# Kernel tuning notes

Measured on AMD Instinct MI355X. Metric: run time of the kernel, lower is better.

## Reference

```python
import jax, jax.numpy as jnp
import numpy as np

N, E, IN, H, G, OUT = 50000, 800000, 128, 128, 64, 10
HEADS, C = 4, 32  # per-head dim = H // HEADS so 4-head concat -> H (keeps chain dims consistent)


def setup_inputs() -> dict:
    key = jax.random.key(0)
    ks = jax.random.split(key, 16)
    p = lambda i, shape: jax.random.normal(ks[i], shape, jnp.float32) * 0.05
    return {
        "x": jax.random.normal(ks[0], (N, IN), jnp.float32),
        "edge_index": jax.random.randint(ks[1], (2, E), 0, N),
        "batch": jnp.sort(jax.random.randint(ks[2], (N,), 0, G)),
        "gcn_W": p(3, (IN, H)), "gcn_b": jnp.zeros((H,), jnp.float32),
        "gat_W": p(4, (H, HEADS * C)),
        "att_src": p(5, (HEADS, C)), "att_dst": p(6, (HEADS, C)),
        "gat_b": jnp.zeros((HEADS * C,), jnp.float32),
        "ec_W1": p(7, (2 * H, 128)), "ec_b1": jnp.zeros((128,), jnp.float32),
        "ec_W2": p(8, (128, H)), "ec_b2": jnp.zeros((H,), jnp.float32),
        "gin_W1": p(9, (H, 128)), "gin_b1": jnp.zeros((128,), jnp.float32),
        "gin_W2": p(10, (128, H)), "gin_b2": jnp.zeros((H,), jnp.float32),
        "gate_W1": p(11, (H, 128)), "gate_b1": jnp.zeros((128,), jnp.float32),
        "gate_W2": p(12, (128, 1)), "gate_b2": jnp.zeros((1,), jnp.float32),
        "fc_W": p(13, (H, OUT)), "fc_b": jnp.zeros((OUT,), jnp.float32),
    }


def reference(x, edge_index, batch, gcn_W, gcn_b, gat_W, att_src, att_dst, gat_b,
              ec_W1, ec_b1, ec_W2, ec_b2, gin_W1, gin_b1, gin_W2, gin_b2,
              gate_W1, gate_b1, gate_W2, gate_b2, fc_W, fc_b):
    src, dst = edge_index[0], edge_index[1]
    loop = jnp.arange(N)
    src_l = jnp.concatenate([src, loop])  # self loops for GCN / GAT
    dst_l = jnp.concatenate([dst, loop])

    deg = jax.ops.segment_sum(jnp.ones_like(dst_l, jnp.float32), dst_l, N)
    dinv = jnp.where(deg > 0, jax.lax.rsqrt(deg), 0.0)
    h = x @ gcn_W
    norm = dinv[src_l] * dinv[dst_l]  # [E+N]
    h = jax.ops.segment_sum(h[src_l] * norm[:, None], dst_l, N) + gcn_b
    h = jax.nn.relu(h)

    # ---- GATConv: 4 heads, per-target edge softmax, concat ----
    g = (h @ gat_W).reshape(N, HEADS, C)
    a_src = (g * att_src).sum(-1)  # [N, HEADS]
    a_dst = (g * att_dst).sum(-1)
    e = jax.nn.leaky_relu(a_src[src_l] + a_dst[dst_l], 0.2)  # [E+N, HEADS]
    e_max = jax.ops.segment_max(e, dst_l, N)
    e = jnp.exp(e - e_max[dst_l])
    e_sum = jax.ops.segment_sum(e, dst_l, N)
    alpha = e / (e_sum[dst_l] + 1e-16)
    h = jax.ops.segment_sum(g[src_l] * alpha[..., None], dst_l, N).reshape(N, HEADS * C) + gat_b
    h = jax.nn.elu(h)

    # ---- EdgeConv: nn([x_i, x_j - x_i]) with max aggregation ----
    msg = jnp.concatenate([h[dst], h[src] - h[dst]], axis=-1)  # [E, 2H]
    msg = jax.nn.relu(msg @ ec_W1 + ec_b1) @ ec_W2 + ec_b2
    agg = jax.ops.segment_max(msg, dst, N)
    h = jax.nn.relu(jnp.where(jnp.isfinite(agg), agg, 0.0))  # isolated nodes -> 0 (PyG scatter-max fill)

    # ---- GINConv (eps=0): nn(x + sum_j x_j) ----
    s = h + jax.ops.segment_sum(h[src], dst, N)
    h = jax.nn.relu(jax.nn.relu(s @ gin_W1 + gin_b1) @ gin_W2 + gin_b2)

    # ---- GlobalAttention pooling: per-graph softmax gating ----
    gate = jax.nn.relu(h @ gate_W1 + gate_b1) @ gate_W2 + gate_b2  # [N, 1]
    gmax = jax.ops.segment_max(gate, batch, G)
    ge = jnp.exp(gate - gmax[batch])
    gsum = jax.ops.segment_sum(ge, batch, G)
    w = ge / (gsum[batch] + 1e-16)
    pooled = jax.ops.segment_sum(w * h, batch, G)  # [G, H]

    out = pooled @ fc_W + fc_b
    return jax.nn.log_softmax(out, axis=1)
```

## Files before the change

### kernel.cpp

```cpp
#include <hip/hip_runtime.h>

#define H 128
#define OUTD 10

typedef short bf16x8 __attribute__((ext_vector_type(8)));
typedef float f32x4 __attribute__((ext_vector_type(4)));

__device__ __forceinline__ unsigned short f2bf(float x) {
  unsigned u = __float_as_uint(x);
  u += 0x7fffu + ((u >> 16) & 1u);
  return (unsigned short)(u >> 16);
}
__device__ __forceinline__ unsigned pack2bf(float a, float b) {
  return (unsigned)f2bf(a) | ((unsigned)f2bf(b) << 16);
}
__device__ __forceinline__ float bf2f(unsigned short u) {
  return __uint_as_float(((unsigned)u) << 16);
}
__device__ __forceinline__ float bflo(unsigned u) { return __uint_as_float(u << 16); }
__device__ __forceinline__ float bfhi(unsigned u) { return __uint_as_float(u & 0xffff0000u); }

__device__ __forceinline__ unsigned fenc(float x) {
  unsigned u = __float_as_uint(x);
  return (u & 0x80000000u) ? ~u : (u | 0x80000000u);
}
__device__ __forceinline__ float fdec(unsigned u) {
  u = (u & 0x80000000u) ? (u & 0x7fffffffu) : ~u;
  return __uint_as_float(u);
}

__global__ void prep_w(const float* __restrict__ gcnW, const float* __restrict__ gatW,
                       const float* __restrict__ ecW1, const float* __restrict__ ecW2,
                       const float* __restrict__ ginW1, const float* __restrict__ ginW2,
                       const float* __restrict__ gtW1, unsigned short* __restrict__ WT) {
  int f = blockIdx.x * 256 + threadIdx.x;
  if (f >= 8 * 16384) return;
  int m = f >> 14, idx = f & 16383;
  int j = idx >> 7, k = idx & 127;
  int src = k * 128 + j;
  float v;
  switch (m) {
    case 0: v = gcnW[src]; break;
    case 1: v = gatW[src]; break;
    case 2: v = ecW1[src] - ecW1[16384 + src]; break;
    case 3: v = ecW1[16384 + src]; break;
    case 4: v = ecW2[src]; break;
    case 5: v = ginW1[src]; break;
    case 6: v = ginW2[src]; break;
    default: v = gtW1[src]; break;
  }
  WT[f] = f2bf(v);
}

template <int IN_BF, int RELU, int BIAS>
__global__ __launch_bounds__(256) void dense_mfma(const void* __restrict__ Xv,
                                                  const unsigned short* __restrict__ WT,
                                                  const float* __restrict__ bias,
                                                  unsigned short* __restrict__ Y, int n) {
  __shared__ unsigned short tile[64][136];
  const int tid = threadIdx.x, lane = tid & 63, wave = tid >> 6;
  const int jl = lane & 15, kg = lane >> 4;
  const int base = blockIdx.x * 64;
  if (base >= n) return;
  const int nr = min(64, n - base);
  if (IN_BF) {
    const uint4* X4 = (const uint4*)Xv;
#pragma unroll
    for (int it = 0; it < 4; ++it) {
      int f = it * 256 + tid, r = f >> 4, q = f & 15;
      if (r < nr) *(uint4*)&tile[r][q * 8] = X4[(size_t)(base + r) * 16 + q];
    }
  } else {
    const float* X = (const float*)Xv;
#pragma unroll
    for (int it = 0; it < 16; ++it) {
      int f = it * 256 + tid, r = f >> 6, kp = f & 63;
      if (r < nr) {
        float2 v = *(const float2*)&X[(size_t)(base + r) * H + 2 * kp];
        *(unsigned*)&tile[r][2 * kp] = pack2bf(v.x, v.y);
      }
    }
  }
  __syncthreads();
  bf16x8 afrag[4];
#pragma unroll
  for (int kk = 0; kk < 4; ++kk)
    afrag[kk] = *(const bf16x8*)&tile[wave * 16 + jl][kk * 32 + kg * 8];
  f32x4 acc[8];
#pragma unroll
  for (int jt = 0; jt < 8; ++jt) {
    f32x4 c = {0.f, 0.f, 0.f, 0.f};
#pragma unroll
    for (int kk = 0; kk < 4; ++kk) {
      bf16x8 bf = *(const bf16x8*)&WT[(size_t)(jt * 16 + jl) * H + kk * 32 + kg * 8];
      c = __builtin_amdgcn_mfma_f32_16x16x32_bf16(afrag[kk], bf, c, 0, 0, 0);
    }
    if (BIAS) {
      float bb = bias[jt * 16 + jl];
#pragma unroll
      for (int r = 0; r < 4; ++r) c[r] += bb;
    }
    if (RELU) {
#pragma unroll
      for (int r = 0; r < 4; ++r) c[r] = fmaxf(c[r], 0.f);
    }
    acc[jt] = c;
  }
  __syncthreads();
#pragma unroll
  for (int jt = 0; jt < 8; ++jt)
#pragma unroll
    for (int r = 0; r < 4; ++r) tile[wave * 16 + kg * 4 + r][jt * 16 + jl] = f2bf(acc[jt][r]);
  __syncthreads();
#pragma unroll
  for (int it = 0; it < 4; ++it) {
    int f = it * 256 + tid, r = f >> 4, q = f & 15;
    if (r < nr) *(uint4*)&Y[(size_t)(base + r) * H + q * 8] = *(const uint4*)&tile[r][q * 8];
  }
}

__global__ __launch_bounds__(256) void dense_dual(const unsigned short* __restrict__ X,
                                                  const unsigned short* __restrict__ WT1,
                                                  const unsigned short* __restrict__ WT2,
                                                  const float* __restrict__ bias2,
                                                  unsigned short* __restrict__ Y1,
                                                  unsigned short* __restrict__ Y2, int n) {
  __shared__ unsigned short tile[64][136];
  const int tid = threadIdx.x, lane = tid & 63, wave = tid >> 6;
  const int jl = lane & 15, kg = lane >> 4;
  const int base = blockIdx.x * 64;
  if (base >= n) return;
  const int nr = min(64, n - base);
  const uint4* X4 = (const uint4*)X;
#pragma unroll
  for (int it = 0; it < 4; ++it) {
    int f = it * 256 + tid, r = f >> 4, q = f & 15;
    if (r < nr) *(uint4*)&tile[r][q * 8] = X4[(size_t)(base + r) * 16 + q];
  }
  __syncthreads();
  bf16x8 afrag[4];
#pragma unroll
  for (int kk = 0; kk < 4; ++kk)
    afrag[kk] = *(const bf16x8*)&tile[wave * 16 + jl][kk * 32 + kg * 8];
  f32x4 acc[8];
#pragma unroll
  for (int jt = 0; jt < 8; ++jt) {
    f32x4 c = {0.f, 0.f, 0.f, 0.f};
#pragma unroll
    for (int kk = 0; kk < 4; ++kk) {
      bf16x8 bf = *(const bf16x8*)&WT1[(size_t)(jt * 16 + jl) * H + kk * 32 + kg * 8];
      c = __builtin_amdgcn_mfma_f32_16x16x32_bf16(afrag[kk], bf, c, 0, 0, 0);
    }
    acc[jt] = c;
  }
  __syncthreads();
#pragma unroll
  for (int jt = 0; jt < 8; ++jt)
#pragma unroll
    for (int r = 0; r < 4; ++r) tile[wave * 16 + kg * 4 + r][jt * 16 + jl] = f2bf(acc[jt][r]);
  __syncthreads();
#pragma unroll
  for (int it = 0; it < 4; ++it) {
    int f = it * 256 + tid, r = f >> 4, q = f & 15;
    if (r < nr) *(uint4*)&Y1[(size_t)(base + r) * H + q * 8] = *(const uint4*)&tile[r][q * 8];
  }
  __syncthreads();
#pragma unroll
  for (int jt = 0; jt < 8; ++jt) {
    f32x4 c = {0.f, 0.f, 0.f, 0.f};
#pragma unroll
    for (int kk = 0; kk < 4; ++kk) {
      bf16x8 bf = *(const bf16x8*)&WT2[(size_t)(jt * 16 + jl) * H + kk * 32 + kg * 8];
      c = __builtin_amdgcn_mfma_f32_16x16x32_bf16(afrag[kk], bf, c, 0, 0, 0);
    }
    float bb = bias2[jt * 16 + jl];
#pragma unroll
    for (int r = 0; r < 4; ++r) c[r] += bb;
    acc[jt] = c;
  }
  __syncthreads();
#pragma unroll
  for (int jt = 0; jt < 8; ++jt)
#pragma unroll
    for (int r = 0; r < 4; ++r) tile[wave * 16 + kg * 4 + r][jt * 16 + jl] = f2bf(acc[jt][r]);
  __syncthreads();
#pragma unroll
  for (int it = 0; it < 4; ++it) {
    int f = it * 256 + tid, r = f >> 4, q = f & 15;
    if (r < nr) *(uint4*)&Y2[(size_t)(base + r) * H + q * 8] = *(const uint4*)&tile[r][q * 8];
  }
}

__global__ __launch_bounds__(256) void dense_chain(const unsigned short* __restrict__ X,
                                                   const unsigned short* __restrict__ WT1,
                                                   const float* __restrict__ b1,
                                                   const unsigned short* __restrict__ WT2,
                                                   const float* __restrict__ b2,
                                                   unsigned short* __restrict__ Y, int n) {
  __shared__ unsigned short tile[64][136];
  const int tid = threadIdx.x, lane = tid & 63, wave = tid >> 6;
  const int jl = lane & 15, kg = lane >> 4;
  const int base = blockIdx.x * 64;
  if (base >= n) return;
  const int nr = min(64, n - base);
  const uint4* X4 = (const uint4*)X;
#pragma unroll
  for (int it = 0; it < 4; ++it) {
    int f = it * 256 + tid, r = f >> 4, q = f & 15;
    if (r < nr) *(uint4*)&tile[r][q * 8] = X4[(size_t)(base + r) * 16 + q];
  }
  __syncthreads();
  bf16x8 af[4];
#pragma unroll
  for (int kk = 0; kk < 4; ++kk) af[kk] = *(const bf16x8*)&tile[wave * 16 + jl][kk * 32 + kg * 8];
  f32x4 acc[8];
#pragma unroll
  for (int jt = 0; jt < 8; ++jt) {
    f32x4 c = {0.f, 0.f, 0.f, 0.f};
#pragma unroll
    for (int kk = 0; kk < 4; ++kk) {
      bf16x8 bf = *(const bf16x8*)&WT1[(size_t)(jt * 16 + jl) * H + kk * 32 + kg * 8];
      c = __builtin_amdgcn_mfma_f32_16x16x32_bf16(af[kk], bf, c, 0, 0, 0);
    }
    float bb = b1[jt * 16 + jl];
#pragma unroll
    for (int r = 0; r < 4; ++r) c[r] = fmaxf(c[r] + bb, 0.f);
    acc[jt] = c;
  }
  __syncthreads();
#pragma unroll
  for (int jt = 0; jt < 8; ++jt)
#pragma unroll
    for (int r = 0; r < 4; ++r) tile[wave * 16 + kg * 4 + r][jt * 16 + jl] = f2bf(acc[jt][r]);
  __syncthreads();
#pragma unroll
  for (int kk = 0; kk < 4; ++kk) af[kk] = *(const bf16x8*)&tile[wave * 16 + jl][kk * 32 + kg * 8];
#pragma unroll
  for (int jt = 0; jt < 8; ++jt) {
    f32x4 c = {0.f, 0.f, 0.f, 0.f};
#pragma unroll
    for (int kk = 0; kk < 4; ++kk) {
      bf16x8 bf = *(const bf16x8*)&WT2[(size_t)(jt * 16 + jl) * H + kk * 32 + kg * 8];
      c = __builtin_amdgcn_mfma_f32_16x16x32_bf16(af[kk], bf, c, 0, 0, 0);
    }
    float bb = b2[jt * 16 + jl];
#pragma unroll
    for (int r = 0; r < 4; ++r) c[r] = fmaxf(c[r] + bb, 0.f);
    acc[jt] = c;
  }
  __syncthreads();
#pragma unroll
  for (int jt = 0; jt < 8; ++jt)
#pragma unroll
    for (int r = 0; r < 4; ++r) tile[wave * 16 + kg * 4 + r][jt * 16 + jl] = f2bf(acc[jt][r]);
  __syncthreads();
#pragma unroll
  for (int it = 0; it < 4; ++it) {
    int f = it * 256 + tid, r = f >> 4, q = f & 15;
    if (r < nr) *(uint4*)&Y[(size_t)(base + r) * H + q * 8] = *(const uint4*)&tile[r][q * 8];
  }
}

__global__ __launch_bounds__(256) void dense_gate(const unsigned short* __restrict__ X,
                                                  const unsigned short* __restrict__ WT,
                                                  const float* __restrict__ b1,
                                                  const float* __restrict__ w2,
                                                  const float* __restrict__ b2,
                                                  float* __restrict__ gate, int n) {
  __shared__ unsigned short tile[64][136];
  const int tid = threadIdx.x, lane = tid & 63, wave = tid >> 6;
  const int jl = lane & 15, kg = lane >> 4;
  const int base = blockIdx.x * 64;
  if (base >= n) return;
  const int nr = min(64, n - base);
  const uint4* X4 = (const uint4*)X;
#pragma unroll
  for (int it = 0; it < 4; ++it) {
    int f = it * 256 + tid, r = f >> 4, q = f & 15;
    if (r < nr) *(uint4*)&tile[r][q * 8] = X4[(size_t)(base + r) * 16 + q];
  }
  __syncthreads();
  bf16x8 af[4];
#pragma unroll
  for (int kk = 0; kk < 4; ++kk) af[kk] = *(const bf16x8*)&tile[wave * 16 + jl][kk * 32 + kg * 8];
  float p0 = 0.f, p1 = 0.f, p2 = 0.f, p3 = 0.f;
#pragma unroll
  for (int jt = 0; jt < 8; ++jt) {
    f32x4 c = {0.f, 0.f, 0.f, 0.f};
#pragma unroll
    for (int kk = 0; kk < 4; ++kk) {
      bf16x8 bf = *(const bf16x8*)&WT[(size_t)(jt * 16 + jl) * H + kk * 32 + kg * 8];
      c = __builtin_amdgcn_mfma_f32_16x16x32_bf16(af[kk], bf, c, 0, 0, 0);
    }
    float bb = b1[jt * 16 + jl];
    float wv = w2[jt * 16 + jl];
    p0 = fmaf(fmaxf(c[0] + bb, 0.f), wv, p0);
    p1 = fmaf(fmaxf(c[1] + bb, 0.f), wv, p1);
    p2 = fmaf(fmaxf(c[2] + bb, 0.f), wv, p2);
    p3 = fmaf(fmaxf(c[3] + bb, 0.f), wv, p3);
  }
#pragma unroll
  for (int off = 1; off <= 8; off <<= 1) {
    p0 += __shfl_xor(p0, off);
    p1 += __shfl_xor(p1, off);
    p2 += __shfl_xor(p2, off);
    p3 += __shfl_xor(p3, off);
  }
  if (jl == 0) {
    float bb2 = b2[0];
    int row = wave * 16 + kg * 4;
    if (row + 0 < nr) gate[base + row + 0] = p0 + bb2;
    if (row + 1 < nr) gate[base + row + 1] = p1 + bb2;
    if (row + 2 < nr) gate[base + row + 2] = p2 + bb2;
    if (row + 3 < nr) gate[base + row + 3] = p3 + bb2;
  }
}

__global__ void zero_int(int* p, int n) {
  int i = blockIdx.x * 256 + threadIdx.x;
  if (i < n) p[i] = 0;
}
__global__ void csr_count(const int* __restrict__ ei, int* __restrict__ cnt, int E) {
  int e = blockIdx.x * 256 + threadIdx.x;
  if (e < E) atomicAdd(&cnt[ei[(size_t)E + e]], 1);
}
__global__ __launch_bounds__(1024) void scan50k(const int* __restrict__ cnt,
                                                int* __restrict__ row_ptr, int n) {
  __shared__ int ls[1024];
  int t = threadIdx.x;
  int chunk = (n + 1023) >> 10;
  int a = t * chunk;
  if (a > n) a = n;
  int b = a + chunk;
  if (b > n) b = n;
  int s = 0;
  for (int i = a; i < b; ++i) s += cnt[i];
  ls[t] = s;
  __syncthreads();
  for (int off = 1; off < 1024; off <<= 1) {
    int v = (t >= off) ? ls[t - off] : 0;
    __syncthreads();
    ls[t] += v;
    __syncthreads();
  }
  int run = (t > 0) ? ls[t - 1] : 0;
  for (int i = a; i < b; ++i) {
    row_ptr[i] = run;
    run += cnt[i];
  }
  if (t == 1023) row_ptr[n] = ls[1023];
}
__global__ void copy_int(const int* __restrict__ a, int* __restrict__ b, int n) {
  int i = blockIdx.x * 256 + threadIdx.x;
  if (i < n) b[i] = a[i];
}
__global__ void csr_fill(const int* __restrict__ ei, int* __restrict__ cursor,
                         int* __restrict__ csr_src, int* __restrict__ csr_dst, int E) {
  int e = blockIdx.x * 256 + threadIdx.x;
  if (e >= E) return;
  int s = ei[e], d = ei[(size_t)E + e];
  int p = atomicAdd(&cursor[d], 1);
  csr_src[p] = s;
  csr_dst[p] = d;
}
__global__ void dinv_kernel(const int* __restrict__ row_ptr, float* __restrict__ dinv, int n) {
  int i = blockIdx.x * 256 + threadIdx.x;
  if (i < n) dinv[i] = rsqrtf((float)(1 + row_ptr[i + 1] - row_ptr[i]));
}
__global__ void fill_u32(unsigned* p, unsigned v, size_t n) {
  size_t i = (size_t)blockIdx.x * 256 + threadIdx.x;
  if (i < n) p[i] = v;
}

__global__ __launch_bounds__(256) void gcn_gather(const unsigned short* __restrict__ h,
                                                  const float* __restrict__ dinv,
                                                  const int* __restrict__ row_ptr,
                                                  const int* __restrict__ csr_src,
                                                  const float* __restrict__ bias,
                                                  unsigned short* __restrict__ out, int n) {
  int node = blockIdx.x * 4 + (threadIdx.x >> 6);
  int lane = threadIdx.x & 63;
  if (node >= n) return;
  const unsigned* hu = (const unsigned*)h;
  float di = dinv[node];
  unsigned v = hu[(size_t)node * 64 + lane];
  float t0 = bflo(v) * di, t1 = bfhi(v) * di;
  int a = row_ptr[node], b = row_ptr[node + 1];
  int e = a;
  for (; e + 8 <= b; e += 8) {
    int sx[8];
#pragma unroll
    for (int i = 0; i < 8; ++i) sx[i] = csr_src[e + i];
    unsigned w[8];
    float dd[8];
#pragma unroll
    for (int i = 0; i < 8; ++i) w[i] = hu[(size_t)sx[i] * 64 + lane];
#pragma unroll
    for (int i = 0; i < 8; ++i) dd[i] = dinv[sx[i]];
#pragma unroll
    for (int i = 0; i < 8; ++i) {
      t0 = fmaf(bflo(w[i]), dd[i], t0);
      t1 = fmaf(bfhi(w[i]), dd[i], t1);
    }
  }
  for (; e < b; ++e) {
    int s = csr_src[e];
    float ds = dinv[s];
    unsigned w = hu[(size_t)s * 64 + lane];
    t0 = fmaf(bflo(w), ds, t0);
    t1 = fmaf(bfhi(w), ds, t1);
  }
  float y0 = fmaxf(fmaf(t0, di, bias[lane * 2]), 0.f);
  float y1 = fmaxf(fmaf(t1, di, bias[lane * 2 + 1]), 0.f);
  ((unsigned*)out)[(size_t)node * 64 + lane] = pack2bf(y0, y1);
}

__global__ void att_pre(const unsigned short* __restrict__ g, const float* __restrict__ attS,
                        const float* __restrict__ attD, float* __restrict__ asrc,
                        float* __restrict__ adst, int n) {
  int t = blockIdx.x * 256 + threadIdx.x;
  if (t >= n * 4) return;
  int i = t >> 2, hd = t & 3;
  const unsigned* gr = (const unsigned*)(g + (size_t)i * H + hd * 32);
  float s1 = 0.f, s2 = 0.f;
#pragma unroll
  for (int p = 0; p < 16; ++p) {
    unsigned u = gr[p];
    float a = bflo(u), b = bfhi(u);
    s1 = fmaf(a, attS[hd * 32 + 2 * p], fmaf(b, attS[hd * 32 + 2 * p + 1], s1));
    s2 = fmaf(a, attD[hd * 32 + 2 * p], fmaf(b, attD[hd * 32 + 2 * p + 1], s2));
  }
  asrc[t] = s1;
  adst[t] = s2;
}

__device__ __forceinline__ float lrelu_exp(float v) {
  v = v > 0.f ? v : 0.2f * v;
  return __expf(v);
}

__global__ __launch_bounds__(256) void gat_gather(const unsigned short* __restrict__ g,
                                                  const float* __restrict__ asrc,
                                                  const float* __restrict__ adst,
                                                  const int* __restrict__ row_ptr,
                                                  const int* __restrict__ csr_src,
                                                  const float* __restrict__ bias,
                                                  unsigned short* __restrict__ out, int n) {
  int node = blockIdx.x * 4 + (threadIdx.x >> 6);
  int lane = threadIdx.x & 63;
  if (node >= n) return;
  const int hd = lane >> 4;
  const unsigned* gu = (const unsigned*)g;
  float adc = adst[node * 4 + hd];
  float w = lrelu_exp(asrc[node * 4 + hd] + adc);
  unsigned u = gu[(size_t)node * 64 + lane];
  float acc0 = w * bflo(u), acc1 = w * bfhi(u), wsum = w;
  int a = row_ptr[node], b = row_ptr[node + 1];
  int e = a;
  for (; e + 4 <= b; e += 4) {
    int s0 = csr_src[e], s1 = csr_src[e + 1], s2 = csr_src[e + 2], s3 = csr_src[e + 3];
    unsigned u0 = gu[(size_t)s0 * 64 + lane], u1 = gu[(size_t)s1 * 64 + lane];
    unsigned u2 = gu[(size_t)s2 * 64 + lane], u3 = gu[(size_t)s3 * 64 + lane];
    float w0 = lrelu_exp(asrc[s0 * 4 + hd] + adc), w1 = lrelu_exp(asrc[s1 * 4 + hd] + adc);
    float w2 = lrelu_exp(asrc[s2 * 4 + hd] + adc), w3 = lrelu_exp(asrc[s3 * 4 + hd] + adc);
    acc0 = fmaf(w0, bflo(u0), acc0);
    acc1 = fmaf(w0, bfhi(u0), acc1);
    acc0 = fmaf(w1, bflo(u1), acc0);
    acc1 = fmaf(w1, bfhi(u1), acc1);
    acc0 = fmaf(w2, bflo(u2), acc0);
    acc1 = fmaf(w2, bfhi(u2), acc1);
    acc0 = fmaf(w3, bflo(u3), acc0);
    acc1 = fmaf(w3, bfhi(u3), acc1);
    wsum += w0 + w1 + w2 + w3;
  }
  for (; e < b; ++e) {
    int s = csr_src[e];
    unsigned us = gu[(size_t)s * 64 + lane];
    float we = lrelu_exp(asrc[s * 4 + hd] + adc);
    acc0 = fmaf(we, bflo(us), acc0);
    acc1 = fmaf(we, bfhi(us), acc1);
    wsum += we;
  }
  float inv = 1.f / (wsum + 1e-16f);
  float r0 = acc0 * inv + bias[2 * lane];
  float r1 = acc1 * inv + bias[2 * lane + 1];
  r0 = r0 > 0.f ? r0 : expm1f(r0);
  r1 = r1 > 0.f ? r1 : expm1f(r1);
  ((unsigned*)out)[(size_t)node * 64 + lane] = pack2bf(r0, r1);
}

__global__ __launch_bounds__(256) void edgeconv_tile(const unsigned short* __restrict__ A,
                                                     const unsigned short* __restrict__ Bm,
                                                     const int* __restrict__ csr_src,
                                                     const int* __restrict__ csr_dst,
                                                     const unsigned short* __restrict__ W2T,
                                                     const float* __restrict__ b2,
                                                     unsigned* __restrict__ hec, int E) {
  __shared__ unsigned short buf[2][64][136];
  __shared__ int dbuf[2][64];
  const int tid = threadIdx.x, lane = tid & 63, wave = tid >> 6;
  const int jl = lane & 15, kg = lane >> 4;
  const int srow = tid >> 2, sq = tid & 3;
  float b2v[8];
#pragma unroll
  for (int jt = 0; jt < 8; ++jt) b2v[jt] = b2[jt * 16 + jl];

  const int tiles = (E + 63) >> 6;
  int t = blockIdx.x;
  if (t >= tiles) return;
  int cur = 0;
  {
    int base = t << 6;
    int ne = min(64, E - base);
    uint2 pk[8];
    if (srow < ne) {
      int d = csr_dst[base + srow], s = csr_src[base + srow];
      const uint2* Ar = (const uint2*)(A + (size_t)d * H + sq * 32);
      const uint2* Br = (const uint2*)(Bm + (size_t)s * H + sq * 32);
#pragma unroll
      for (int i = 0; i < 8; ++i) {
        uint2 va = Ar[i], vb = Br[i];
        pk[i].x = pack2bf(fmaxf(bflo(va.x) + bflo(vb.x), 0.f), fmaxf(bfhi(va.x) + bfhi(vb.x), 0.f));
        pk[i].y = pack2bf(fmaxf(bflo(va.y) + bflo(vb.y), 0.f), fmaxf(bfhi(va.y) + bfhi(vb.y), 0.f));
      }
    } else {
#pragma unroll
      for (int i = 0; i < 8; ++i) pk[i] = {0u, 0u};
    }
#pragma unroll
    for (int i = 0; i < 8; ++i) *(uint2*)&buf[0][srow][sq * 32 + i * 4] = pk[i];
    if (sq == 0) dbuf[0][srow] = (srow < ne) ? csr_dst[base + srow] : -1;
  }
  __syncthreads();

  for (; t < tiles; t += gridDim.x) {
    const int nt = t + gridDim.x;
    const bool havenext = nt < tiles;
    uint2 pk[8];
    if (havenext) {
      int base = nt << 6;
      int ne = min(64, E - base);
      if (srow < ne) {
        int d = csr_dst[base + srow], s = csr_src[base + srow];
        const uint2* Ar = (const uint2*)(A + (size_t)d * H + sq * 32);
        const uint2* Br = (const uint2*)(Bm + (size_t)s * H + sq * 32);
#pragma unroll
        for (int i = 0; i < 8; ++i) {
          uint2 va = Ar[i], vb = Br[i];
          pk[i].x =
              pack2bf(fmaxf(bflo(va.x) + bflo(vb.x), 0.f), fmaxf(bfhi(va.x) + bfhi(vb.x), 0.f));
          pk[i].y =
              pack2bf(fmaxf(bflo(va.y) + bflo(vb.y), 0.f), fmaxf(bfhi(va.y) + bfhi(vb.y), 0.f));
        }
      } else {
#pragma unroll
        for (int i = 0; i < 8; ++i) pk[i] = {0u, 0u};
      }
    }
    bf16x8 af[4];
#pragma unroll
    for (int kk = 0; kk < 4; ++kk)
      af[kk] = *(const bf16x8*)&buf[cur][wave * 16 + jl][kk * 32 + kg * 8];
    const int r0 = wave * 16 + kg * 4;
    const int d0 = dbuf[cur][r0 + 0], d1 = dbuf[cur][r0 + 1];
    const int d2 = dbuf[cur][r0 + 2], d3 = dbuf[cur][r0 + 3];
#pragma unroll
    for (int jt = 0; jt < 8; ++jt) {
      f32x4 c = {0.f, 0.f, 0.f, 0.f};
#pragma unroll
      for (int kk = 0; kk < 4; ++kk) {
        bf16x8 wf = *(const bf16x8*)&W2T[(size_t)(jt * 16 + jl) * H + kk * 32 + kg * 8];
        c = __builtin_amdgcn_mfma_f32_16x16x32_bf16(af[kk], wf, c, 0, 0, 0);
      }
      const int col = jt * 16 + jl;
      int cd = d0;
      float m = c[0];
      if (d1 != cd) {
        if (cd >= 0) atomicMax(&hec[(size_t)cd * H + col], fenc(m + b2v[jt]));
        cd = d1;
        m = c[1];
      } else
        m = fmaxf(m, c[1]);
      if (d2 != cd) {
        if (cd >= 0) atomicMax(&hec[(size_t)cd * H + col], fenc(m + b2v[jt]));
        cd = d2;
        m = c[2];
      } else
        m = fmaxf(m, c[2]);
      if (d3 != cd) {
        if (cd >= 0) atomicMax(&hec[(size_t)cd * H + col], fenc(m + b2v[jt]));
        cd = d3;
        m = c[3];
      } else
        m = fmaxf(m, c[3]);
      if (cd >= 0) atomicMax(&hec[(size_t)cd * H + col], fenc(m + b2v[jt]));
    }
    if (havenext) {
      int base = nt << 6;
      int ne = min(64, E - base);
#pragma unroll
      for (int i = 0; i < 8; ++i) *(uint2*)&buf[cur ^ 1][srow][sq * 32 + i * 4] = pk[i];
      if (sq == 0) dbuf[cur ^ 1][srow] = (srow < ne) ? csr_dst[base + srow] : -1;
    }
    __syncthreads();
    cur ^= 1;
  }
}

__global__ __launch_bounds__(256) void gin_gather(const unsigned* __restrict__ hec,
                                                  const int* __restrict__ row_ptr,
                                                  const int* __restrict__ csr_src,
                                                  unsigned short* __restrict__ out, int n) {
  int node = blockIdx.x * 4 + (threadIdx.x >> 6);
  int lane = threadIdx.x & 63;
  if (node >= n) return;
  uint2 v = *(const uint2*)&hec[(size_t)node * H + lane * 2];
  float t0 = fdec(v.x), t1 = fdec(v.y);
  int a = row_ptr[node], b = row_ptr[node + 1];
  int e = a;
  for (; e + 4 <= b; e += 4) {
    int s0 = csr_src[e], s1 = csr_src[e + 1], s2 = csr_src[e + 2], s3 = csr_src[e + 3];
    uint2 w0 = *(const uint2*)&hec[(size_t)s0 * H + lane * 2];
    uint2 w1 = *(const uint2*)&hec[(size_t)s1 * H + lane * 2];
    uint2 w2 = *(const uint2*)&hec[(size_t)s2 * H + lane * 2];
    uint2 w3 = *(const uint2*)&hec[(size_t)s3 * H + lane * 2];
    t0 += fdec(w0.x) + fdec(w1.x) + fdec(w2.x) + fdec(w3.x);
    t1 += fdec(w0.y) + fdec(w1.y) + fdec(w2.y) + fdec(w3.y);
  }
  for (; e < b; ++e) {
    int s = csr_src[e];
    uint2 w = *(const uint2*)&hec[(size_t)s * H + lane * 2];
    t0 += fdec(w.x);
    t1 += fdec(w.y);
  }
  ((unsigned*)out)[(size_t)node * 64 + lane] = pack2bf(t0, t1);
}

__global__ void starts_kernel(const int* __restrict__ batch, int* __restrict__ starts, int n,
                              int G) {
  int i = blockIdx.x * 256 + threadIdx.x;
  if (i >= n) return;
  int b = batch[i];
  int bp = (i == 0) ? -1 : batch[i - 1];
  for (int g = bp + 1; g <= b; ++g) starts[g] = i;
  if (i == n - 1)
    for (int g = b + 1; g <= G; ++g) starts[g] = n;
}
__global__ __launch_bounds__(256) void pool_fused(float* __restrict__ gate,
                                                  const unsigned short* __restrict__ h4,
                                                  const int* __restrict__ starts,
                                                  const float* __restrict__ fcW,
                                                  const float* __restrict__ fcB,
                                                  float* __restrict__ out) {
  __shared__ float red[256];
  __shared__ float pl[128];
  int g = blockIdx.x, t = threadIdx.x;
  int s0 = starts[g], s1 = starts[g + 1];
  float m = -1e30f;
  for (int i = s0 + t; i < s1; i += 256) m = fmaxf(m, gate[i]);
  red[t] = m;
  __syncthreads();
  for (int off = 128; off; off >>= 1) {
    if (t < off) red[t] = fmaxf(red[t], red[t + off]);
    __syncthreads();
  }
  m = red[0];
  __syncthreads();
  float sm = 0.f;
  for (int i = s0 + t; i < s1; i += 256) {
    float ge = __expf(gate[i] - m);
    gate[i] = ge;
    sm += ge;
  }
  red[t] = sm;
  __syncthreads();
  for (int off = 128; off; off >>= 1) {
    if (t < off) red[t] += red[t + off];
    __syncthreads();
  }
  float inv = 1.f / (red[0] + 1e-16f);
  __syncthreads();
  int c = t & 127, half = t >> 7;
  float acc = 0.f;
  for (int i = s0 + half; i < s1; i += 2) acc = fmaf(gate[i], bf2f(h4[(size_t)i * H + c]), acc);
  red[t] = acc;
  __syncthreads();
  if (t < 128) pl[t] = (red[t] + red[t + 128]) * inv;
  __syncthreads();
  if (t < OUTD) {
    float o = fcB[t];
    for (int k = 0; k < 128; ++k) o = fmaf(pl[k], fcW[k * OUTD + t], o);
    red[t] = o;
  }
  __syncthreads();
  if (t == 0) {
    float mm = -1e30f;
    for (int j = 0; j < OUTD; ++j) mm = fmaxf(mm, red[j]);
    float s = 0.f;
    for (int j = 0; j < OUTD; ++j) s += __expf(red[j] - mm);
    float l = logf(s);
    for (int j = 0; j < OUTD; ++j) out[g * OUTD + j] = red[j] - mm - l;
  }
}

extern "C" void kernel_launch(void* const* d_in, const int* in_sizes, int n_in, void* d_out,
                              int out_size, void* d_ws, size_t ws_size, hipStream_t stream) {
  const float* x = (const float*)d_in[0];
  const int* ei = (const int*)d_in[1];
  const int* batch = (const int*)d_in[2];
  const float* gcnW = (const float*)d_in[3];
  const float* gcnB = (const float*)d_in[4];
  const float* gatW = (const float*)d_in[5];
  const float* attS = (const float*)d_in[6];
  const float* attD = (const float*)d_in[7];
  const float* gatB = (const float*)d_in[8];
  const float* ecW1 = (const float*)d_in[9];
  const float* ecB1 = (const float*)d_in[10];
  const float* ecW2 = (const float*)d_in[11];
  const float* ecB2 = (const float*)d_in[12];
  const float* ginW1 = (const float*)d_in[13];
  const float* ginB1 = (const float*)d_in[14];
  const float* ginW2 = (const float*)d_in[15];
  const float* ginB2 = (const float*)d_in[16];
  const float* gtW1 = (const float*)d_in[17];
  const float* gtB1 = (const float*)d_in[18];
  const float* gtW2 = (const float*)d_in[19];
  const float* gtB2 = (const float*)d_in[20];
  const float* fcW = (const float*)d_in[21];
  const float* fcB = (const float*)d_in[22];

  const int N = in_sizes[0] / H;
  const int E = in_sizes[1] / 2;
  const int G = out_size / OUTD;
  const size_t NH = (size_t)N * H;

  auto align16 = [](char* p) { return (char*)(((uintptr_t)p + 15) & ~(uintptr_t)15); };
  char* p = (char*)d_ws;
  unsigned* hec = (unsigned*)p;      p += NH * 4;
  float* dinv = (float*)p;           p += (size_t)N * 4;
  float* asrc = (float*)p;           p += (size_t)4 * N * 4;
  float* adst = (float*)p;           p += (size_t)4 * N * 4;
  float* gate = (float*)p;           p += (size_t)N * 4;
  int* starts = (int*)p;             p += (size_t)(G + 1) * 4;
  int* cnt = (int*)p;                p += (size_t)N * 4;
  int* row_ptr = (int*)p;            p += (size_t)(N + 1) * 4;
  int* cursor = (int*)p;             p += (size_t)N * 4;
  int* csr_src = (int*)p;            p += (size_t)E * 4;
  int* csr_dst = (int*)p;            p += (size_t)E * 4;
  p = align16(p);
  unsigned short* WT = (unsigned short*)p;  p += (size_t)8 * 16384 * 2;
  p = align16(p);
  unsigned short* T0 = (unsigned short*)p;  p += NH * 2;
  p = align16(p);
  unsigned short* T1 = (unsigned short*)p;  p += NH * 2;
  p = align16(p);
  unsigned short* T2 = (unsigned short*)p;  p += NH * 2;

  const unsigned short* gcnT = WT;
  const unsigned short* gatT = WT + 16384;
  const unsigned short* WaT = WT + 2 * 16384;
  const unsigned short* WbT = WT + 3 * 16384;
  const unsigned short* W2T = WT + 4 * 16384;
  const unsigned short* gin1T = WT + 5 * 16384;
  const unsigned short* gin2T = WT + 6 * 16384;
  const unsigned short* gt1T = WT + 7 * 16384;

  const int gN = (N + 255) / 256;
  const int gNH = (int)((NH + 255) / 256);
  const int gE = (E + 255) / 256;
  const int gDense = (N + 63) / 64;
  const int gW4 = (N + 3) / 4;

  prep_w<<<(8 * 16384 + 255) / 256, 256, 0, stream>>>(gcnW, gatW, ecW1, ecW2, ginW1, ginW2,
                                                      gtW1, WT);
  zero_int<<<gN, 256, 0, stream>>>(cnt, N);
  csr_count<<<gE, 256, 0, stream>>>(ei, cnt, E);
  scan50k<<<1, 1024, 0, stream>>>(cnt, row_ptr, N);
  copy_int<<<gN, 256, 0, stream>>>(row_ptr, cursor, N);
  csr_fill<<<gE, 256, 0, stream>>>(ei, cursor, csr_src, csr_dst, E);
  dinv_kernel<<<gN, 256, 0, stream>>>(row_ptr, dinv, N);

  dense_mfma<0, 0, 0><<<gDense, 256, 0, stream>>>(x, gcnT, nullptr, T0, N);
  gcn_gather<<<gW4, 256, 0, stream>>>(T0, dinv, row_ptr, csr_src, gcnB, T1, N);

  dense_mfma<1, 0, 0><<<gDense, 256, 0, stream>>>(T1, gatT, nullptr, T2, N);
  att_pre<<<(N * 4 + 255) / 256, 256, 0, stream>>>(T2, attS, attD, asrc, adst, N);
  gat_gather<<<gW4, 256, 0, stream>>>(T2, asrc, adst, row_ptr, csr_src, gatB, T0, N);

  dense_dual<<<gDense, 256, 0, stream>>>(T0, WaT, WbT, ecB1, T1, T2, N);
  fill_u32<<<gNH, 256, 0, stream>>>(hec, 0x80000000u, NH);
  edgeconv_tile<<<2048, 256, 0, stream>>>(T1, T2, csr_src, csr_dst, W2T, ecB2, hec, E);

  gin_gather<<<gW4, 256, 0, stream>>>(hec, row_ptr, csr_src, T0, N);
  dense_chain<<<gDense, 256, 0, stream>>>(T0, gin1T, ginB1, gin2T, ginB2, T2, N);

  dense_gate<<<gDense, 256, 0, stream>>>(T2, gt1T, gtB1, gtW2, gtB2, gate, N);
  starts_kernel<<<gN, 256, 0, stream>>>(batch, starts, N, G);
  pool_fused<<<G, 256, 0, stream>>>(gate, T2, starts, fcW, fcB, (float*)d_out);
}
```

Measured before the change: 817.0 us.

## Decode EdgeConv max to bf16 before GIN gather, deepen gather unrolls, reorder edgeconv sync

Adds an ec_decode pass that converts the order-encoded fp32 EdgeConv max buffer into bf16 once. GIN gather then reads 256-byte bf16 rows instead of 512-byte fp32 rows per neighbor, roughly halving random-gather traffic. GAT and GIN gathers now unroll by 8 to keep more loads in flight. In edgeconv_tile, the next tile's LDS staging and barrier move ahead of the atomicMax epilogue, and LDS row padding changes to 140, at the cost of one extra kernel launch and an extra bf16 rounding before the sum.

```diff
diff --git a/kernel.cpp b/kernel.cpp
--- a/kernel.cpp
+++ b/kernel.cpp
@@ -457,21 +457,22 @@
   float acc0 = w * bflo(u), acc1 = w * bfhi(u), wsum = w;
   int a = row_ptr[node], b = row_ptr[node + 1];
   int e = a;
-  for (; e + 4 <= b; e += 4) {
-    int s0 = csr_src[e], s1 = csr_src[e + 1], s2 = csr_src[e + 2], s3 = csr_src[e + 3];
-    unsigned u0 = gu[(size_t)s0 * 64 + lane], u1 = gu[(size_t)s1 * 64 + lane];
-    unsigned u2 = gu[(size_t)s2 * 64 + lane], u3 = gu[(size_t)s3 * 64 + lane];
-    float w0 = lrelu_exp(asrc[s0 * 4 + hd] + adc), w1 = lrelu_exp(asrc[s1 * 4 + hd] + adc);
-    float w2 = lrelu_exp(asrc[s2 * 4 + hd] + adc), w3 = lrelu_exp(asrc[s3 * 4 + hd] + adc);
-    acc0 = fmaf(w0, bflo(u0), acc0);
-    acc1 = fmaf(w0, bfhi(u0), acc1);
-    acc0 = fmaf(w1, bflo(u1), acc0);
-    acc1 = fmaf(w1, bfhi(u1), acc1);
-    acc0 = fmaf(w2, bflo(u2), acc0);
-    acc1 = fmaf(w2, bfhi(u2), acc1);
-    acc0 = fmaf(w3, bflo(u3), acc0);
-    acc1 = fmaf(w3, bfhi(u3), acc1);
-    wsum += w0 + w1 + w2 + w3;
+  for (; e + 8 <= b; e += 8) {
+    int sx[8];
+#pragma unroll
+    for (int i = 0; i < 8; ++i) sx[i] = csr_src[e + i];
+    unsigned uu[8];
+#pragma unroll
+    for (int i = 0; i < 8; ++i) uu[i] = gu[(size_t)sx[i] * 64 + lane];
+    float ww[8];
+#pragma unroll
+    for (int i = 0; i < 8; ++i) ww[i] = lrelu_exp(asrc[sx[i] * 4 + hd] + adc);
+#pragma unroll
+    for (int i = 0; i < 8; ++i) {
+      acc0 = fmaf(ww[i], bflo(uu[i]), acc0);
+      acc1 = fmaf(ww[i], bfhi(uu[i]), acc1);
+      wsum += ww[i];
+    }
   }
   for (; e < b; ++e) {
     int s = csr_src[e];
@@ -496,7 +497,7 @@
                                                      const unsigned short* __restrict__ W2T,
                                                      const float* __restrict__ b2,
                                                      unsigned* __restrict__ hec, int E) {
-  __shared__ unsigned short buf[2][64][136];
+  __shared__ unsigned short buf[2][64][140];
   __shared__ int dbuf[2][64];
   const int tid = threadIdx.x, lane = tid & 63, wave = tid >> 6;
   const int jl = lane & 15, kg = lane >> 4;
@@ -564,6 +565,7 @@
     const int r0 = wave * 16 + kg * 4;
     const int d0 = dbuf[cur][r0 + 0], d1 = dbuf[cur][r0 + 1];
     const int d2 = dbuf[cur][r0 + 2], d3 = dbuf[cur][r0 + 3];
+    f32x4 acc[8];
 #pragma unroll
     for (int jt = 0; jt < 8; ++jt) {
       f32x4 c = {0.f, 0.f, 0.f, 0.f};
@@ -572,7 +574,20 @@
         bf16x8 wf = *(const bf16x8*)&W2T[(size_t)(jt * 16 + jl) * H + kk * 32 + kg * 8];
         c = __builtin_amdgcn_mfma_f32_16x16x32_bf16(af[kk], wf, c, 0, 0, 0);
       }
+      acc[jt] = c;
+    }
+    if (havenext) {
+      int base = nt << 6;
+      int ne = min(64, E - base);
+#pragma unroll
+      for (int i = 0; i < 8; ++i) *(uint2*)&buf[cur ^ 1][srow][sq * 32 + i * 4] = pk[i];
+      if (sq == 0) dbuf[cur ^ 1][srow] = (srow < ne) ? csr_dst[base + srow] : -1;
+    }
+    __syncthreads();
+#pragma unroll
+    for (int jt = 0; jt < 8; ++jt) {
       const int col = jt * 16 + jl;
+      f32x4 c = acc[jt];
       int cd = d0;
       float m = c[0];
       if (d1 != cd) {
@@ -595,43 +610,49 @@
         m = fmaxf(m, c[3]);
       if (cd >= 0) atomicMax(&hec[(size_t)cd * H + col], fenc(m + b2v[jt]));
     }
-    if (havenext) {
-      int base = nt << 6;
-      int ne = min(64, E - base);
-#pragma unroll
-      for (int i = 0; i < 8; ++i) *(uint2*)&buf[cur ^ 1][srow][sq * 32 + i * 4] = pk[i];
-      if (sq == 0) dbuf[cur ^ 1][srow] = (srow < ne) ? csr_dst[base + srow] : -1;
-    }
-    __syncthreads();
     cur ^= 1;
   }
 }
 
-__global__ __launch_bounds__(256) void gin_gather(const unsigned* __restrict__ hec,
+__global__ void ec_decode(const unsigned* __restrict__ hec, unsigned short* __restrict__ out,
+                          size_t half) {
+  size_t i = (size_t)blockIdx.x * 256 + threadIdx.x;
+  if (i < half) {
+    uint2 v = *(const uint2*)&hec[i * 2];
+    ((unsigned*)out)[i] = pack2bf(fdec(v.x), fdec(v.y));
+  }
+}
+
+__global__ __launch_bounds__(256) void gin_gather(const unsigned short* __restrict__ h,
                                                   const int* __restrict__ row_ptr,
                                                   const int* __restrict__ csr_src,
                                                   unsigned short* __restrict__ out, int n) {
   int node = blockIdx.x * 4 + (threadIdx.x >> 6);
   int lane = threadIdx.x & 63;
   if (node >= n) return;
-  uint2 v = *(const uint2*)&hec[(size_t)node * H + lane * 2];
-  float t0 = fdec(v.x), t1 = fdec(v.y);
+  const unsigned* hu = (const unsigned*)h;
+  unsigned v = hu[(size_t)node * 64 + lane];
+  float t0 = bflo(v), t1 = bfhi(v);
   int a = row_ptr[node], b = row_ptr[node + 1];
   int e = a;
-  for (; e + 4 <= b; e += 4) {
-    int s0 = csr_src[e], s1 = csr_src[e + 1], s2 = csr_src[e + 2], s3 = csr_src[e + 3];
-    uint2 w0 = *(const uint2*)&hec[(size_t)s0 * H + lane * 2];
-    uint2 w1 = *(const uint2*)&hec[(size_t)s1 * H + lane * 2];
-    uint2 w2 = *(const uint2*)&hec[(size_t)s2 * H + lane * 2];
-    uint2 w3 = *(const uint2*)&hec[(size_t)s3 * H + lane * 2];
-    t0 += fdec(w0.x) + fdec(w1.x) + fdec(w2.x) + fdec(w3.x);
-    t1 += fdec(w0.y) + fdec(w1.y) + fdec(w2.y) + fdec(w3.y);
+  for (; e + 8 <= b; e += 8) {
+    int sx[8];
+#pragma unroll
+    for (int i = 0; i < 8; ++i) sx[i] = csr_src[e + i];
+    unsigned w[8];
+#pragma unroll
+    for (int i = 0; i < 8; ++i) w[i] = hu[(size_t)sx[i] * 64 + lane];
+#pragma unroll
+    for (int i = 0; i < 8; ++i) {
+      t0 += bflo(w[i]);
+      t1 += bfhi(w[i]);
+    }
   }
   for (; e < b; ++e) {
     int s = csr_src[e];
-    uint2 w = *(const uint2*)&hec[(size_t)s * H + lane * 2];
-    t0 += fdec(w.x);
-    t1 += fdec(w.y);
+    unsigned w = hu[(size_t)s * 64 + lane];
+    t0 += bflo(w);
+    t1 += bfhi(w);
   }
   ((unsigned*)out)[(size_t)node * 64 + lane] = pack2bf(t0, t1);
 }
@@ -790,9 +811,10 @@
   dense_dual<<<gDense, 256, 0, stream>>>(T0, WaT, WbT, ecB1, T1, T2, N);
   fill_u32<<<gNH, 256, 0, stream>>>(hec, 0x80000000u, NH);
   edgeconv_tile<<<2048, 256, 0, stream>>>(T1, T2, csr_src, csr_dst, W2T, ecB2, hec, E);
-
-  gin_gather<<<gW4, 256, 0, stream>>>(hec, row_ptr, csr_src, T0, N);
-  dense_chain<<<gDense, 256, 0, stream>>>(T0, gin1T, ginB1, gin2T, ginB2, T2, N);
+  ec_decode<<<(int)((NH / 2 + 255) / 256), 256, 0, stream>>>(hec, T0, NH / 2);
+
+  gin_gather<<<gW4, 256, 0, stream>>>(T0, row_ptr, csr_src, T1, N);
+  dense_chain<<<gDense, 256, 0, stream>>>(T1, gin1T, ginB1, gin2T, ginB2, T2, N);
 
   dense_gate<<<gDense, 256, 0, stream>>>(T2, gt1T, gtB1, gtW2, gtB2, gate, N);
   starts_kernel<<<gN, 256, 0, stream>>>(batch, starts, N, G);
```

Result: no change. 813.6 us (-0.4%).
